# Optimization experiments

Hardware: AMD Instinct MI355X
Metric: run time of the kernel (lower is better)

Reference implementation:

```python
import jax, jax.numpy as jnp
import numpy as np

EMB = 4096
NUM_EXPERTS = 64
TOP_K = 2
TOKENS = 16384


def setup_inputs() -> dict:
    key = jax.random.key(0)
    kx, kw, kb = jax.random.split(key, 3)
    x = jax.random.normal(kx, (TOKENS, EMB), dtype=jnp.float32)
    # nn.Linear(emb_size, num_experts): weight [num_experts, emb], bias [num_experts]
    W = jax.random.normal(kw, (NUM_EXPERTS, EMB), dtype=jnp.float32) / np.sqrt(EMB)
    b = jax.random.normal(kb, (NUM_EXPERTS,), dtype=jnp.float32) * 0.01
    return {"x": x, "W": W, "b": b}


def reference(x, W, b):
    # logits = x @ W.T + b  -> [tokens, num_experts]
    logits = jnp.einsum("td,ed->te", x, W) + b
    topk_val, topk_idx = jax.lax.top_k(logits, TOP_K)  # [tokens, k]
    probs = jax.nn.softmax(topk_val, axis=-1)
    return (topk_idx, probs)
```

## Files before the change

kernel.cpp:

```cpp
#include <hip/hip_runtime.h>

#define TOKENS 16384
#define EMB 4096
#define NEXP 64
#define BK 32

typedef __attribute__((ext_vector_type(8))) short short8;
typedef __attribute__((ext_vector_type(4))) float f32x4;
typedef __attribute__((ext_vector_type(4))) unsigned short ush4;

#define WP_USHORTS (3 * NEXP * EMB)
#define WP_FLOATS  (WP_USHORTS / 2)

__device__ __forceinline__ void gl_lds16(const void* g, void* lds) {
    __builtin_amdgcn_global_load_lds(
        (const __attribute__((address_space(1))) void*)g,
        (__attribute__((address_space(3))) void*)lds, 16, 0, 0);
}

__device__ __forceinline__ void split3(float x, unsigned short& h,
                                       unsigned short& m, unsigned short& l) {
    unsigned u = __float_as_uint(x);
    unsigned r = u + 0x7FFFu + ((u >> 16) & 1u);
    float hF = __uint_as_float(r & 0xFFFF0000u);
    h = (unsigned short)(r >> 16);
    float r1 = x - hF;
    unsigned u1 = __float_as_uint(r1);
    float mF = __uint_as_float(u1 & 0xFFFF0000u);
    m = (unsigned short)(u1 >> 16);
    float r2 = r1 - mF;
    l = (unsigned short)(__float_as_uint(r2) >> 16);
}

__device__ __forceinline__ void split3_pair(float x0, float x1,
        unsigned& hw, unsigned& mw, unsigned& lw) {
    unsigned u0 = __float_as_uint(x0), u1 = __float_as_uint(x1);
    unsigned r0 = u0 + 0x7FFFu + ((u0 >> 16) & 1u);
    unsigned r1 = u1 + 0x7FFFu + ((u1 >> 16) & 1u);
    hw = __builtin_amdgcn_perm(r1, r0, 0x07060302u);
    float s0 = x0 - __uint_as_float(r0 & 0xFFFF0000u);
    float s1 = x1 - __uint_as_float(r1 & 0xFFFF0000u);
    unsigned v0 = __float_as_uint(s0), v1 = __float_as_uint(s1);
    mw = __builtin_amdgcn_perm(v1, v0, 0x07060302u);
    float t0 = s0 - __uint_as_float(v0 & 0xFFFF0000u);
    float t1 = s1 - __uint_as_float(v1 & 0xFFFF0000u);
    lw = __builtin_amdgcn_perm(__float_as_uint(t1), __float_as_uint(t0), 0x07060302u);
}

__device__ __forceinline__ void build_frags(const float4& a0, const float4& a1,
        short8& H, short8& M, short8& L) {
    union { short8 v; unsigned u[4]; } h_, m_, l_;
    split3_pair(a0.x, a0.y, h_.u[0], m_.u[0], l_.u[0]);
    split3_pair(a0.z, a0.w, h_.u[1], m_.u[1], l_.u[1]);
    split3_pair(a1.x, a1.y, h_.u[2], m_.u[2], l_.u[2]);
    split3_pair(a1.z, a1.w, h_.u[3], m_.u[3], l_.u[3]);
    H = h_.v; M = m_.v; L = l_.v;
}

__global__ __launch_bounds__(256) void split_w(const float* __restrict__ W,
                                               unsigned short* __restrict__ Wp) {
    const int i = (blockIdx.x * 256 + threadIdx.x) * 4;
    const float4 v = *reinterpret_cast<const float4*>(W + i);
    ush4 h, m, l;
#pragma unroll
    for (int e = 0; e < 4; ++e) {
        unsigned short he, me, le;
        split3(reinterpret_cast<const float*>(&v)[e], he, me, le);
        h[e] = he; m[e] = me; l[e] = le;
    }
    *reinterpret_cast<ush4*>(Wp + i) = h;
    *reinterpret_cast<ush4*>(Wp + NEXP * EMB + i) = m;
    *reinterpret_cast<ush4*>(Wp + 2 * NEXP * EMB + i) = l;
}

#define MFMA_BLOCK(BUFC, AH0, AM0, AL0, AH1, AM1, AL1)                          \
    _Pragma("unroll")                                                           \
    for (int et = 0; et < 4; ++et) {                                            \
        const unsigned short* bp = &sB[BUFC][et * 16 + lr][lo * 8];             \
        const short8 bH = *reinterpret_cast<const short8*>(bp);                 \
        const short8 bM = *reinterpret_cast<const short8*>(bp + 64 * BK);       \
        const short8 bL = *reinterpret_cast<const short8*>(bp + 128 * BK);      \
        accH[0][et] = __builtin_amdgcn_mfma_f32_16x16x32_bf16(AH0, bH, accH[0][et], 0, 0, 0); \
        accL[0][et] = __builtin_amdgcn_mfma_f32_16x16x32_bf16(AH0, bM, accL[0][et], 0, 0, 0); \
        accL[0][et] = __builtin_amdgcn_mfma_f32_16x16x32_bf16(AM0, bH, accL[0][et], 0, 0, 0); \
        accL[0][et] = __builtin_amdgcn_mfma_f32_16x16x32_bf16(AM0, bM, accL[0][et], 0, 0, 0); \
        accL[0][et] = __builtin_amdgcn_mfma_f32_16x16x32_bf16(AH0, bL, accL[0][et], 0, 0, 0); \
        accL[0][et] = __builtin_amdgcn_mfma_f32_16x16x32_bf16(AL0, bH, accL[0][et], 0, 0, 0); \
        accH[1][et] = __builtin_amdgcn_mfma_f32_16x16x32_bf16(AH1, bH, accH[1][et], 0, 0, 0); \
        accL[1][et] = __builtin_amdgcn_mfma_f32_16x16x32_bf16(AH1, bM, accL[1][et], 0, 0, 0); \
        accL[1][et] = __builtin_amdgcn_mfma_f32_16x16x32_bf16(AM1, bH, accL[1][et], 0, 0, 0); \
        accL[1][et] = __builtin_amdgcn_mfma_f32_16x16x32_bf16(AM1, bM, accL[1][et], 0, 0, 0); \
        accL[1][et] = __builtin_amdgcn_mfma_f32_16x16x32_bf16(AH1, bL, accL[1][et], 0, 0, 0); \
        accL[1][et] = __builtin_amdgcn_mfma_f32_16x16x32_bf16(AL1, bH, accL[1][et], 0, 0, 0); \
    }

#define BODY_MAIN(KS, AC, BUFC) do {                                            \
    asm volatile("s_waitcnt vmcnt(4)" ::: "memory");                            \
    __builtin_amdgcn_s_barrier();                                               \
    _Pragma("unroll")                                                           \
    for (int p = 0; p < 3; ++p)                                                 \
        gl_lds16(gb[p] + ((KS) + 1) * BK, &sB[(BUFC) ^ 1][48 * w + 16 * p][0]); \
    short8 aH0, aM0, aL0, aH1, aM1, aL1;                                        \
    build_frags(AC[0][0], AC[0][1], aH0, aM0, aL0);                             \
    build_frags(AC[1][0], AC[1][1], aH1, aM1, aL1);                             \
    _Pragma("unroll")                                                           \
    for (int ti = 0; ti < 2; ++ti) {                                            \
        AC[ti][0] = *reinterpret_cast<const float4*>(ax[ti] + ((KS) + 2) * BK);     \
        AC[ti][1] = *reinterpret_cast<const float4*>(ax[ti] + ((KS) + 2) * BK + 4); \
    }                                                                           \
    __builtin_amdgcn_sched_barrier(0);                                          \
    MFMA_BLOCK(BUFC, aH0, aM0, aL0, aH1, aM1, aL1)                              \
} while (0)

template<int S>
__global__ __launch_bounds__(256, 3) void router_mfma(
    const float* __restrict__ x, const unsigned short* __restrict__ Wp,
    float* __restrict__ part)
{
    constexpr int KPER = EMB / S;
    constexpr int NCH  = KPER / BK;

    __shared__ unsigned short sB[2][192][BK];

    const int t  = threadIdx.x;
    const int w  = t >> 6;
    const int l  = t & 63;
    const int lr = l & 15;
    const int lo = l >> 4;
    const int tok0 = blockIdx.x * 128 + w * 32;
    const int kb   = blockIdx.y * KPER;

    const float* ax[2];
    ax[0] = x + (size_t)(tok0 + lr) * EMB + kb + lo * 8;
    ax[1] = x + (size_t)(tok0 + 16 + lr) * EMB + kb + lo * 8;

    const unsigned short* gb[3];
#pragma unroll
    for (int p = 0; p < 3; ++p)
        gb[p] = Wp + (size_t)(48 * w + 16 * p + (l >> 2)) * EMB + kb + 8 * (l & 3);

    f32x4 accH[2][4], accL[2][4];
#pragma unroll
    for (int ti = 0; ti < 2; ++ti)
#pragma unroll
        for (int et = 0; et < 4; ++et) {
            accH[ti][et] = (f32x4){0.f, 0.f, 0.f, 0.f};
            accL[ti][et] = (f32x4){0.f, 0.f, 0.f, 0.f};
        }

    float4 aA[2][2], aB[2][2];
#pragma unroll
    for (int ti = 0; ti < 2; ++ti) {
        aA[ti][0] = *reinterpret_cast<const float4*>(ax[ti]);
        aA[ti][1] = *reinterpret_cast<const float4*>(ax[ti] + 4);
    }
#pragma unroll
    for (int p = 0; p < 3; ++p)
        gl_lds16(gb[p], &sB[0][48 * w + 16 * p][0]);
#pragma unroll
    for (int ti = 0; ti < 2; ++ti) {
        aB[ti][0] = *reinterpret_cast<const float4*>(ax[ti] + BK);
        aB[ti][1] = *reinterpret_cast<const float4*>(ax[ti] + BK + 4);
    }

#pragma unroll 1
    for (int kt = 0; kt < NCH - 2; kt += 2) {
        BODY_MAIN(kt, aA, 0);
        BODY_MAIN(kt + 1, aB, 1);
    }

    {
        asm volatile("s_waitcnt vmcnt(4)" ::: "memory");
        __builtin_amdgcn_s_barrier();
#pragma unroll
        for (int p = 0; p < 3; ++p)
            gl_lds16(gb[p] + (NCH - 1) * BK, &sB[1][48 * w + 16 * p][0]);
        short8 aH0, aM0, aL0, aH1, aM1, aL1;
        build_frags(aA[0][0], aA[0][1], aH0, aM0, aL0);
        build_frags(aA[1][0], aA[1][1], aH1, aM1, aL1);
        MFMA_BLOCK(0, aH0, aM0, aL0, aH1, aM1, aL1)
    }
    {
        asm volatile("s_waitcnt vmcnt(0)" ::: "memory");
        __builtin_amdgcn_s_barrier();
        short8 aH0, aM0, aL0, aH1, aM1, aL1;
        build_frags(aB[0][0], aB[0][1], aH0, aM0, aL0);
        build_frags(aB[1][0], aB[1][1], aH1, aM1, aL1);
        MFMA_BLOCK(1, aH0, aM0, aL0, aH1, aM1, aL1)
    }

#pragma unroll
    for (int ti = 0; ti < 2; ++ti)
#pragma unroll
        for (int et = 0; et < 4; ++et)
#pragma unroll
            for (int j = 0; j < 4; ++j) {
                const int tok = tok0 + ti * 16 + lo * 4 + j;
                part[((size_t)blockIdx.y * TOKENS + tok) * NEXP + et * 16 + lr]
                    = accH[ti][et][j] + accL[ti][et][j];
            }
}

template<int S>
__global__ __launch_bounds__(256) void reduce_topk(
    const float* __restrict__ part, const float* __restrict__ b,
    float* __restrict__ out)
{
    __shared__ double sv[64][4][2];
    __shared__ int    si[64][4][2];
    const int t    = threadIdx.x;
    const int p4   = t & 3;
    const int slot = t >> 2;
    const int tok  = blockIdx.x * 64 + slot;

    double v[16];
#pragma unroll
    for (int j = 0; j < 16; ++j) v[j] = 0.0;
    for (int s = 0; s < S; ++s) {
        const float4* pp = reinterpret_cast<const float4*>(
            part + ((size_t)s * TOKENS + tok) * NEXP + (p4 << 4));
#pragma unroll
        for (int q = 0; q < 4; ++q) {
            const float4 f = pp[q];
            v[4 * q + 0] += (double)f.x;
            v[4 * q + 1] += (double)f.y;
            v[4 * q + 2] += (double)f.z;
            v[4 * q + 3] += (double)f.w;
        }
    }
#pragma unroll
    for (int j = 0; j < 16; ++j) v[j] += (double)b[(p4 << 4) + j];

    double v1 = -1e300, v2 = -1e300; int i1 = 0, i2 = 0;
#pragma unroll
    for (int j = 0; j < 16; ++j) {
        const int e = (p4 << 4) + j;
        if (v[j] > v1)      { v2 = v1; i2 = i1; v1 = v[j]; i1 = e; }
        else if (v[j] > v2) { v2 = v[j]; i2 = e; }
    }
    sv[slot][p4][0] = v1; sv[slot][p4][1] = v2;
    si[slot][p4][0] = i1; si[slot][p4][1] = i2;
    __syncthreads();

    if (p4 == 0) {
        double m1 = -1e300, m2 = -1e300; int j1 = 0, j2 = 0;
#pragma unroll
        for (int p = 0; p < 4; ++p)
#pragma unroll
            for (int r = 0; r < 2; ++r) {
                const double vv = sv[slot][p][r]; const int ii = si[slot][p][r];
                if (vv > m1)      { m2 = m1; j2 = j1; m1 = vv; j1 = ii; }
                else if (vv > m2) { m2 = vv; j2 = ii; }
            }
        const float e2  = expf((float)(m2 - m1));
        const float inv = 1.0f / (1.0f + e2);
        out[2 * tok]     = (float)j1;
        out[2 * tok + 1] = (float)j2;
        out[2 * TOKENS + 2 * tok]     = inv;
        out[2 * TOKENS + 2 * tok + 1] = e2 * inv;
    }
}

extern "C" void kernel_launch(void* const* d_in, const int* in_sizes, int n_in,
                              void* d_out, int out_size, void* d_ws, size_t ws_size,
                              hipStream_t stream) {
    const float* x = (const float*)d_in[0];
    const float* W = (const float*)d_in[1];
    const float* b = (const float*)d_in[2];
    float* out = (float*)d_out;
    unsigned short* Wp = (unsigned short*)d_ws;
    float* part = (float*)d_ws + WP_FLOATS;

    split_w<<<dim3(NEXP * EMB / 1024), dim3(256), 0, stream>>>(W, Wp);

    const size_t base = (size_t)WP_FLOATS * 4;
    const size_t per  = (size_t)TOKENS * NEXP * 4;
    if (ws_size >= base + 8 * per) {
        router_mfma<8><<<dim3(TOKENS / 128, 8), dim3(256), 0, stream>>>(x, Wp, part);
        reduce_topk<8><<<dim3(TOKENS / 64), dim3(256), 0, stream>>>(part, b, out);
    } else if (ws_size >= base + 4 * per) {
        router_mfma<4><<<dim3(TOKENS / 128, 4), dim3(256), 0, stream>>>(x, Wp, part);
        reduce_topk<4><<<dim3(TOKENS / 64), dim3(256), 0, stream>>>(part, b, out);
    } else {
        router_mfma<2><<<dim3(TOKENS / 128, 2), dim3(256), 0, stream>>>(x, Wp, part);
        reduce_topk<2><<<dim3(TOKENS / 64), dim3(256), 0, stream>>>(part, b, out);
    }
}
```

Measured before the change: 85.04 us.

## Fuse split-K router GEMM with top-k reduction in one kernel via LDS

Replaces the two-kernel split-K GEMM plus reduce_topk with one 512-thread kernel. Inside it, four warp-pair groups each take a quarter of K for the same 64 tokens, leave their partial logits in LDS, and then reduce them with the bias and pick the top-2 in the same block. This removes the global partial-logit buffer's write and read-back and one kernel launch. In exchange, each block now fetches the full split weight tile, which doubles weight traffic through L2. LDS use also grows to roughly 98KB per block, so fewer waves are resident per CU.

```diff
diff --git a/kernel.cpp b/kernel.cpp
--- a/kernel.cpp
+++ b/kernel.cpp
@@ -4,6 +4,9 @@
 #define EMB 4096
 #define NEXP 64
 #define BK 32
+#define KSP 4
+#define KPER (EMB / KSP)
+#define NCH (KPER / BK)
 
 typedef __attribute__((ext_vector_type(8))) short short8;
 typedef __attribute__((ext_vector_type(4))) float f32x4;
@@ -76,7 +79,7 @@
 #define MFMA_BLOCK(BUFC, AH0, AM0, AL0, AH1, AM1, AL1)                          \
     _Pragma("unroll")                                                           \
     for (int et = 0; et < 4; ++et) {                                            \
-        const unsigned short* bp = &sB[BUFC][et * 16 + lr][lo * 8];             \
+        const unsigned short* bp = &sB[g][BUFC][et * 16 + lr][lo * 8];          \
         const short8 bH = *reinterpret_cast<const short8*>(bp);                 \
         const short8 bM = *reinterpret_cast<const short8*>(bp + 64 * BK);       \
         const short8 bL = *reinterpret_cast<const short8*>(bp + 128 * BK);      \
@@ -94,12 +97,14 @@
         accL[1][et] = __builtin_amdgcn_mfma_f32_16x16x32_bf16(AL1, bH, accL[1][et], 0, 0, 0); \
     }
 
-#define BODY_MAIN(KS, AC, BUFC) do {                                            \
+#define BODY(KS, AC, BUFC) do {                                                 \
     asm volatile("s_waitcnt vmcnt(4)" ::: "memory");                            \
     __builtin_amdgcn_s_barrier();                                               \
     _Pragma("unroll")                                                           \
-    for (int p = 0; p < 3; ++p)                                                 \
-        gl_lds16(gb[p] + ((KS) + 1) * BK, &sB[(BUFC) ^ 1][48 * w + 16 * p][0]); \
+    for (int p = 0; p < 6; ++p)                                                 \
+        gl_lds16(gb[p] + ((KS) + 1) * BK,                                       \
+                 &sB[g][(BUFC) ^ 1][16 * (6 * h + p)][0]);                      \
+    __builtin_amdgcn_sched_barrier(0);                                          \
     short8 aH0, aM0, aL0, aH1, aM1, aL1;                                        \
     build_frags(AC[0][0], AC[0][1], aH0, aM0, aL0);                             \
     build_frags(AC[1][0], AC[1][1], aH1, aM1, aL1);                             \
@@ -112,32 +117,31 @@
     MFMA_BLOCK(BUFC, aH0, aM0, aL0, aH1, aM1, aL1)                              \
 } while (0)
 
-template<int S>
-__global__ __launch_bounds__(256, 3) void router_mfma(
+__global__ __launch_bounds__(512) void router_fused(
     const float* __restrict__ x, const unsigned short* __restrict__ Wp,
-    float* __restrict__ part)
+    const float* __restrict__ b, float* __restrict__ out)
 {
-    constexpr int KPER = EMB / S;
-    constexpr int NCH  = KPER / BK;
-
-    __shared__ unsigned short sB[2][192][BK];
+    __shared__ unsigned short sB[KSP][2][192][BK];
 
     const int t  = threadIdx.x;
     const int w  = t >> 6;
     const int l  = t & 63;
+    const int g  = w >> 1;
+    const int h  = w & 1;
     const int lr = l & 15;
     const int lo = l >> 4;
-    const int tok0 = blockIdx.x * 128 + w * 32;
-    const int kb   = blockIdx.y * KPER;
+    const int tokB = blockIdx.x * 64;
+    const int tok0 = tokB + h * 32;
+    const int kb   = g * KPER;
 
     const float* ax[2];
     ax[0] = x + (size_t)(tok0 + lr) * EMB + kb + lo * 8;
-    ax[1] = x + (size_t)(tok0 + 16 + lr) * EMB + kb + lo * 8;
-
-    const unsigned short* gb[3];
-#pragma unroll
-    for (int p = 0; p < 3; ++p)
-        gb[p] = Wp + (size_t)(48 * w + 16 * p + (l >> 2)) * EMB + kb + 8 * (l & 3);
+    ax[1] = ax[0] + (size_t)16 * EMB;
+
+    const unsigned short* gb[6];
+#pragma unroll
+    for (int p = 0; p < 6; ++p)
+        gb[p] = Wp + (size_t)(16 * (6 * h + p) + (l >> 2)) * EMB + kb + 8 * (l & 3);
 
     f32x4 accH[2][4], accL[2][4];
 #pragma unroll
@@ -154,27 +158,30 @@
         aA[ti][0] = *reinterpret_cast<const float4*>(ax[ti]);
         aA[ti][1] = *reinterpret_cast<const float4*>(ax[ti] + 4);
     }
-#pragma unroll
-    for (int p = 0; p < 3; ++p)
-        gl_lds16(gb[p], &sB[0][48 * w + 16 * p][0]);
+    __builtin_amdgcn_sched_barrier(0);
+#pragma unroll
+    for (int p = 0; p < 6; ++p)
+        gl_lds16(gb[p], &sB[g][0][16 * (6 * h + p)][0]);
+    __builtin_amdgcn_sched_barrier(0);
 #pragma unroll
     for (int ti = 0; ti < 2; ++ti) {
         aB[ti][0] = *reinterpret_cast<const float4*>(ax[ti] + BK);
         aB[ti][1] = *reinterpret_cast<const float4*>(ax[ti] + BK + 4);
     }
+    __builtin_amdgcn_sched_barrier(0);
 
 #pragma unroll 1
     for (int kt = 0; kt < NCH - 2; kt += 2) {
-        BODY_MAIN(kt, aA, 0);
-        BODY_MAIN(kt + 1, aB, 1);
-    }
-
+        BODY(kt, aA, 0);
+        BODY(kt + 1, aB, 1);
+    }
     {
         asm volatile("s_waitcnt vmcnt(4)" ::: "memory");
         __builtin_amdgcn_s_barrier();
 #pragma unroll
-        for (int p = 0; p < 3; ++p)
-            gl_lds16(gb[p] + (NCH - 1) * BK, &sB[1][48 * w + 16 * p][0]);
+        for (int p = 0; p < 6; ++p)
+            gl_lds16(gb[p] + (NCH - 1) * BK, &sB[g][1][16 * (6 * h + p)][0]);
+        __builtin_amdgcn_sched_barrier(0);
         short8 aH0, aM0, aL0, aH1, aM1, aL1;
         build_frags(aA[0][0], aA[0][1], aH0, aM0, aL0);
         build_frags(aA[1][0], aA[1][1], aH1, aM1, aL1);
@@ -189,75 +196,67 @@
         MFMA_BLOCK(1, aH0, aM0, aL0, aH1, aM1, aL1)
     }
 
+    __syncthreads();
+    float* logits = reinterpret_cast<float*>(&sB[0][0][0][0]);
 #pragma unroll
     for (int ti = 0; ti < 2; ++ti)
 #pragma unroll
         for (int et = 0; et < 4; ++et)
 #pragma unroll
             for (int j = 0; j < 4; ++j) {
-                const int tok = tok0 + ti * 16 + lo * 4 + j;
-                part[((size_t)blockIdx.y * TOKENS + tok) * NEXP + et * 16 + lr]
+                const int ltok = h * 32 + ti * 16 + lo * 4 + j;
+                logits[(g * 64 + ltok) * 65 + et * 16 + lr]
                     = accH[ti][et][j] + accL[ti][et][j];
             }
-}
-
-template<int S>
-__global__ __launch_bounds__(256) void reduce_topk(
-    const float* __restrict__ part, const float* __restrict__ b,
-    float* __restrict__ out)
-{
-    __shared__ double sv[64][4][2];
-    __shared__ int    si[64][4][2];
-    const int t    = threadIdx.x;
-    const int p4   = t & 3;
-    const int slot = t >> 2;
-    const int tok  = blockIdx.x * 64 + slot;
-
-    double v[16];
-#pragma unroll
-    for (int j = 0; j < 16; ++j) v[j] = 0.0;
-    for (int s = 0; s < S; ++s) {
-        const float4* pp = reinterpret_cast<const float4*>(
-            part + ((size_t)s * TOKENS + tok) * NEXP + (p4 << 4));
-#pragma unroll
-        for (int q = 0; q < 4; ++q) {
-            const float4 f = pp[q];
-            v[4 * q + 0] += (double)f.x;
-            v[4 * q + 1] += (double)f.y;
-            v[4 * q + 2] += (double)f.z;
-            v[4 * q + 3] += (double)f.w;
-        }
-    }
-#pragma unroll
-    for (int j = 0; j < 16; ++j) v[j] += (double)b[(p4 << 4) + j];
+    __syncthreads();
+
+    double* sv = reinterpret_cast<double*>(logits + KSP * 64 * 65);
+    int*    si = reinterpret_cast<int*>(sv + 64 * 8 * 2);
+
+    const int tok  = t >> 3;
+    const int part = t & 7;
+    double v[8];
+#pragma unroll
+    for (int j = 0; j < 8; ++j) v[j] = 0.0;
+#pragma unroll
+    for (int gg = 0; gg < KSP; ++gg)
+#pragma unroll
+        for (int j = 0; j < 8; ++j)
+            v[j] += (double)logits[(gg * 64 + tok) * 65 + part * 8 + j];
+#pragma unroll
+    for (int j = 0; j < 8; ++j) v[j] += (double)b[part * 8 + j];
 
     double v1 = -1e300, v2 = -1e300; int i1 = 0, i2 = 0;
 #pragma unroll
-    for (int j = 0; j < 16; ++j) {
-        const int e = (p4 << 4) + j;
+    for (int j = 0; j < 8; ++j) {
+        const int e = part * 8 + j;
         if (v[j] > v1)      { v2 = v1; i2 = i1; v1 = v[j]; i1 = e; }
         else if (v[j] > v2) { v2 = v[j]; i2 = e; }
     }
-    sv[slot][p4][0] = v1; sv[slot][p4][1] = v2;
-    si[slot][p4][0] = i1; si[slot][p4][1] = i2;
+    sv[(tok * 8 + part) * 2 + 0] = v1;
+    sv[(tok * 8 + part) * 2 + 1] = v2;
+    si[(tok * 8 + part) * 2 + 0] = i1;
+    si[(tok * 8 + part) * 2 + 1] = i2;
     __syncthreads();
 
-    if (p4 == 0) {
+    if (part == 0) {
         double m1 = -1e300, m2 = -1e300; int j1 = 0, j2 = 0;
 #pragma unroll
-        for (int p = 0; p < 4; ++p)
+        for (int p = 0; p < 8; ++p)
 #pragma unroll
             for (int r = 0; r < 2; ++r) {
-                const double vv = sv[slot][p][r]; const int ii = si[slot][p][r];
+                const double vv = sv[(tok * 8 + p) * 2 + r];
+                const int    ii = si[(tok * 8 + p) * 2 + r];
                 if (vv > m1)      { m2 = m1; j2 = j1; m1 = vv; j1 = ii; }
                 else if (vv > m2) { m2 = vv; j2 = ii; }
             }
         const float e2  = expf((float)(m2 - m1));
         const float inv = 1.0f / (1.0f + e2);
-        out[2 * tok]     = (float)j1;
-        out[2 * tok + 1] = (float)j2;
-        out[2 * TOKENS + 2 * tok]     = inv;
-        out[2 * TOKENS + 2 * tok + 1] = e2 * inv;
+        const int gt = tokB + tok;
+        out[2 * gt]     = (float)j1;
+        out[2 * gt + 1] = (float)j2;
+        out[2 * TOKENS + 2 * gt]     = inv;
+        out[2 * TOKENS + 2 * gt + 1] = e2 * inv;
     }
 }
 
@@ -269,20 +268,7 @@
     const float* b = (const float*)d_in[2];
     float* out = (float*)d_out;
     unsigned short* Wp = (unsigned short*)d_ws;
-    float* part = (float*)d_ws + WP_FLOATS;
 
     split_w<<<dim3(NEXP * EMB / 1024), dim3(256), 0, stream>>>(W, Wp);
-
-    const size_t base = (size_t)WP_FLOATS * 4;
-    const size_t per  = (size_t)TOKENS * NEXP * 4;
-    if (ws_size >= base + 8 * per) {
-        router_mfma<8><<<dim3(TOKENS / 128, 8), dim3(256), 0, stream>>>(x, Wp, part);
-        reduce_topk<8><<<dim3(TOKENS / 64), dim3(256), 0, stream>>>(part, b, out);
-    } else if (ws_size >= base + 4 * per) {
-        router_mfma<4><<<dim3(TOKENS / 128, 4), dim3(256), 0, stream>>>(x, Wp, part);
-        reduce_topk<4><<<dim3(TOKENS / 64), dim3(256), 0, stream>>>(part, b, out);
-    } else {
-        router_mfma<2><<<dim3(TOKENS / 128, 2), dim3(256), 0, stream>>>(x, Wp, part);
-        reduce_topk<2><<<dim3(TOKENS / 64), dim3(256), 0, stream>>>(part, b, out);
-    }
-}
+    router_fused<<<dim3(TOKENS / 64), dim3(512), 0, stream>>>(x, Wp, b, out);
+}
```

Measured after the change: 76.48 us (median of 2 runs). 1.11x faster.
